# Optimization experiments

Hardware: AMD Instinct MI355X
Metric: run time of the kernel (lower is better)

Reference implementation:

```python
import jax, jax.numpy as jnp
import numpy as np

PS = 8  # window_size
LOCAL = 16  # split channels

def conv1x1(x, w, b):
    return jnp.einsum('oi,bihw->bohw', w, x) + b[None, :, None, None]

def dynamic_local(x, w1, b1, w2, b2, k):
    # x: (B, C, H, W); dynamic per-(batch,channel) depthwise conv with generated kernels
    B, C, H, W = x.shape
    pooled = x.mean((2, 3))                      # (B, C) adaptive avg pool to 1x1
    h = jax.nn.relu(pooled @ w1.T + b1)
    kern = (h @ w2.T + b2).reshape(B, C, k, k)   # per-sample depthwise kernels
    def per_batch(xb, kb):
        return jax.lax.conv_general_dilated(
            xb[None], kb[:, None], (1, 1), 'SAME',
            feature_group_count=C,
            dimension_numbers=('NCHW', 'OIHW', 'NCHW'))[0]
    return jax.vmap(per_batch)(x, kern)

def channel_layernorm(x, w, b, eps=1e-6):
    # LayerNorm over channel dim (torch module's non-channels_last path)
    u = x.mean(1, keepdims=True)
    s = ((x - u) ** 2).mean(1, keepdims=True)
    xn = (x - u) / jnp.sqrt(s + eps)
    return w[None, :, None, None] * xn + b[None, :, None, None]

def fsas(x, hid_w, hid_b, dw_w, dw_b, ln_w, ln_b, out_w, out_b):
    hidden = conv1x1(x, hid_w, hid_b)
    mid = hidden.shape[1]
    dw = jax.lax.conv_general_dilated(
        hidden, dw_w[:, None], (1, 1), 'SAME',
        feature_group_count=mid,
        dimension_numbers=('NCHW', 'OIHW', 'NCHW')) + dw_b[None, :, None, None]
    q, k, v = jnp.split(dw, 3, axis=1)
    B, C, H, W = q.shape
    def patch(t):
        # (B,C,H,W) -> (B,C,H/ps,W/ps,ps,ps)
        return t.reshape(B, C, H // PS, PS, W // PS, PS).transpose(0, 1, 2, 4, 3, 5)
    qf = jnp.fft.rfft2(patch(q))
    kf = jnp.fft.rfft2(patch(k))
    out = jnp.fft.irfft2(qf * kf, s=(PS, PS))
    out = out.transpose(0, 1, 2, 4, 3, 5).reshape(B, C, H, W)
    out = channel_layernorm(out, ln_w, ln_b)
    return conv1x1(v * out, out_w, out_b)


def setup_inputs() -> dict:
    key = jax.random.key(0)
    ks = jax.random.split(key, 12)
    s = 0.02
    return {
        'x': jax.random.normal(ks[0], (4, 64, 256, 256), jnp.float32),
        'dl1_w1': jax.random.normal(ks[1], (16, 16), jnp.float32) * s,
        'dl1_b1': jnp.zeros((16,), jnp.float32),
        'dl1_w2': jax.random.normal(ks[2], (144, 16), jnp.float32) * s,
        'dl1_b2': jnp.zeros((144,), jnp.float32),
        'dl2_w1': jax.random.normal(ks[3], (16, 16), jnp.float32) * s,
        'dl2_b1': jnp.zeros((16,), jnp.float32),
        'dl2_w2': jax.random.normal(ks[4], (400, 16), jnp.float32) * s,
        'dl2_b2': jnp.zeros((400,), jnp.float32),
        'fs_hid_w': jax.random.normal(ks[5], (144, 48), jnp.float32) * s,
        'fs_hid_b': jnp.zeros((144,), jnp.float32),
        'fs_dw_w': jax.random.normal(ks[6], (144, 3, 3), jnp.float32) * s,
        'fs_dw_b': jnp.zeros((144,), jnp.float32),
        'fs_ln_w': jnp.ones((48,), jnp.float32),
        'fs_ln_b': jnp.zeros((48,), jnp.float32),
        'fs_out_w': jax.random.normal(ks[7], (48, 48), jnp.float32) * s,
        'fs_out_b': jnp.zeros((48,), jnp.float32),
        'last_w': jax.random.normal(ks[8], (64, 64), jnp.float32) * s,
        'last_b': jnp.zeros((64,), jnp.float32),
    }


def reference(x, dl1_w1, dl1_b1, dl1_w2, dl1_b2, dl2_w1, dl2_b1, dl2_w2, dl2_b2,
              fs_hid_w, fs_hid_b, fs_dw_w, fs_dw_b, fs_ln_w, fs_ln_b,
              fs_out_w, fs_out_b, last_w, last_b):
    x1, x2 = x[:, :LOCAL], x[:, LOCAL:]
    x1 = dynamic_local(x1, dl1_w1, dl1_b1, dl1_w2, dl1_b2, 3)
    x1 = dynamic_local(x1, dl2_w1, dl2_b1, dl2_w2, dl2_b2, 5)
    x2 = fsas(x2, fs_hid_w, fs_hid_b, fs_dw_w, fs_dw_b, fs_ln_w, fs_ln_b, fs_out_w, fs_out_b)
    return conv1x1(jnp.concatenate([x1, x2], axis=1), last_w, last_b)
```

## Files before the change

kernel.cpp:

```cpp
#include <hip/hip_runtime.h>

typedef _Float16 h2 __attribute__((ext_vector_type(2)));
typedef _Float16 h4 __attribute__((ext_vector_type(4)));
typedef _Float16 h8 __attribute__((ext_vector_type(8)));
typedef float f4 __attribute__((ext_vector_type(4)));
typedef unsigned int u32;
typedef u32 u32x2 __attribute__((ext_vector_type(2)));
typedef u32 u32x4 __attribute__((ext_vector_type(4)));

__device__ __forceinline__ h2 bch2(u32 v) { return __builtin_bit_cast(h2, v); }

__device__ __forceinline__ float warpsum(float v) {
    for (int off = 32; off > 0; off >>= 1) v += __shfl_down(v, off);
    return v;
}

__device__ __forceinline__ int sswz(int p, int k) {
    return p * 64 + ((((k >> 3) ^ (p >> 3)) & 7) << 3) + (k & 7);
}

__global__ __launch_bounds__(256) void k_prep(const float* __restrict__ hid_w,
                                              const float* __restrict__ out_w,
                                              const float* __restrict__ last_w,
                                              const float* __restrict__ out_b,
                                              const float* __restrict__ last_b,
                                              _Float16* __restrict__ hwH,
                                              _Float16* __restrict__ lwC,
                                              float* __restrict__ bias_comb) {
    int t = blockIdx.x * 256 + threadIdx.x;
    int stride = gridDim.x * 256;
    for (int i = t; i < 10368; i += stride) {
        int n = i / 72, k = i - n * 72;
        hwH[i] = (k < 48) ? (_Float16)hid_w[n * 48 + k] : (_Float16)0.f;
    }
    for (int i = t; i < 4096; i += stride) {
        int n = i >> 6, k = i & 63;
        float v;
        if (k < 16) v = last_w[n * 64 + k];
        else {
            v = 0.f;
            for (int o = 0; o < 48; ++o) v += last_w[n * 64 + 16 + o] * out_w[o * 48 + (k - 16)];
        }
        lwC[i] = (_Float16)v;
    }
    for (int n = t; n < 64; n += stride) {
        float v = last_b[n];
        for (int o = 0; o < 48; ++o) v += last_w[n * 64 + 16 + o] * out_b[o];
        bias_comb[n] = v;
    }
}

__global__ __launch_bounds__(256) void k_pool(const float* __restrict__ x, float* __restrict__ pooled1) {
    int bid = blockIdx.x;
    int b = bid >> 4, c = bid & 15;
    const float* base = x + (size_t)(b * 64 + c) * 65536;
    float s = 0.f;
    for (int i = threadIdx.x; i < 16384; i += 256) {
        float4 v = ((const float4*)base)[i];
        s += v.x + v.y + v.z + v.w;
    }
    __shared__ float red[4];
    s = warpsum(s);
    if ((threadIdx.x & 63) == 0) red[threadIdx.x >> 6] = s;
    __syncthreads();
    if (threadIdx.x == 0) pooled1[bid] = (red[0] + red[1] + red[2] + red[3]) * (1.f / 65536.f);
}

__global__ __launch_bounds__(256) void k_kern1(const float* __restrict__ pooled1,
                                               const float* __restrict__ w1, const float* __restrict__ b1,
                                               const float* __restrict__ w2, const float* __restrict__ b2,
                                               float* __restrict__ kern1) {
    __shared__ float h[64];
    int t = threadIdx.x;
    if (t < 64) {
        int b = t >> 4, j = t & 15;
        float a = b1[j];
        for (int i = 0; i < 16; ++i) a += pooled1[b * 16 + i] * w1[j * 16 + i];
        h[t] = fmaxf(a, 0.f);
    }
    __syncthreads();
    for (int i = t; i < 576; i += 256) {
        int b = i / 144, o = i - b * 144;
        float a = b2[o];
        for (int j = 0; j < 16; ++j) a += h[b * 16 + j] * w2[o * 16 + j];
        kern1[i] = a;
    }
}

__global__ __launch_bounds__(256) void k_dw3(const float* __restrict__ x,
                                             const float* __restrict__ kern1,
                                             float* __restrict__ y1, float* __restrict__ rowsum) {
    __shared__ float tile[10][258];
    __shared__ float red[8][4];
    int bid = blockIdx.x;
    int rb = bid & 31, bc = bid >> 5;
    int b = bc >> 4, c = bc & 15;
    int row0 = rb << 3;
    int col = threadIdx.x;
    const float* xc = x + ((size_t)(b * 64 + c) << 16);
#pragma unroll
    for (int j = 0; j < 10; ++j) {
        int r = row0 - 1 + j;
        tile[j][col + 1] = ((unsigned)r < 256u) ? xc[(r << 8) + col] : 0.f;
    }
    if (col < 10) { tile[col][0] = 0.f; tile[col][257] = 0.f; }
    const float* k9 = kern1 + b * 144 + c * 9;
    float kk[9];
#pragma unroll
    for (int i = 0; i < 9; ++i) kk[i] = k9[i];
    __syncthreads();
#pragma unroll
    for (int j = 0; j < 8; ++j) {
        float acc = 0.f;
#pragma unroll
        for (int dy = 0; dy < 3; ++dy)
#pragma unroll
            for (int dx = 0; dx < 3; ++dx)
                acc += kk[dy * 3 + dx] * tile[j + dy][col + dx];
        y1[((size_t)bc << 16) + ((row0 + j) << 8) + col] = acc;
        float s = warpsum(acc);
        if ((col & 63) == 0) red[j][col >> 6] = s;
    }
    __syncthreads();
    if (col < 8) rowsum[bc * 256 + row0 + col] = red[col][0] + red[col][1] + red[col][2] + red[col][3];
}

__global__ __launch_bounds__(256) void k_kern2(const float* __restrict__ rowsum,
                                               const float* __restrict__ w1, const float* __restrict__ b1,
                                               const float* __restrict__ w2, const float* __restrict__ b2,
                                               float* __restrict__ kern2) {
    __shared__ float ps[256];
    __shared__ float p2[64];
    __shared__ float h[64];
    int t = threadIdx.x;
    {
        int pair = t >> 2, seg = t & 3;
        const float* rs = rowsum + pair * 256 + seg * 64;
        float s = 0.f;
        for (int j = 0; j < 64; ++j) s += rs[j];
        ps[t] = s;
    }
    __syncthreads();
    if (t < 64) p2[t] = (ps[t * 4] + ps[t * 4 + 1] + ps[t * 4 + 2] + ps[t * 4 + 3]) * (1.f / 65536.f);
    __syncthreads();
    if (t < 64) {
        int b = t >> 4, j = t & 15;
        float a = b1[j];
        for (int i = 0; i < 16; ++i) a += p2[b * 16 + i] * w1[j * 16 + i];
        h[t] = fmaxf(a, 0.f);
    }
    __syncthreads();
    for (int i = t; i < 1600; i += 256) {
        int b = i / 400, o = i - b * 400;
        float a = b2[o];
        for (int j = 0; j < 16; ++j) a += h[b * 16 + j] * w2[o * 16 + j];
        kern2[i] = a;
    }
}

__global__ __launch_bounds__(256) void k_dw5(const float* __restrict__ y1,
                                             const float* __restrict__ kern2,
                                             float* __restrict__ x1o) {
    __shared__ float tile[12][260];
    int bid = blockIdx.x;
    int rb = bid & 31, bc = bid >> 5;
    int b = bc >> 4, c = bc & 15;
    int row0 = rb << 3;
    int col = threadIdx.x;
    const float* yc = y1 + ((size_t)bc << 16);
#pragma unroll
    for (int j = 0; j < 12; ++j) {
        int r = row0 - 2 + j;
        tile[j][col + 2] = ((unsigned)r < 256u) ? yc[(r << 8) + col] : 0.f;
    }
    if (col < 12) { tile[col][0] = 0.f; tile[col][1] = 0.f; tile[col][258] = 0.f; tile[col][259] = 0.f; }
    const float* k25 = kern2 + b * 400 + c * 25;
    float kk[25];
#pragma unroll
    for (int i = 0; i < 25; ++i) kk[i] = k25[i];
    __syncthreads();
#pragma unroll
    for (int j = 0; j < 8; ++j) {
        float acc = 0.f;
#pragma unroll
        for (int dy = 0; dy < 5; ++dy)
#pragma unroll
            for (int dx = 0; dx < 5; ++dx)
                acc += kk[dy * 5 + dx] * tile[j + dy][col + dx];
        x1o[((size_t)bc << 16) + ((row0 + j) << 8) + col] = acc;
    }
}

__global__ __launch_bounds__(512, 6) void k_fsas(const float* __restrict__ x,
                                                 const _Float16* __restrict__ hwH, const float* __restrict__ hid_b,
                                                 const float* __restrict__ dw_w, const float* __restrict__ dw_b,
                                                 const float* __restrict__ ln_w, const float* __restrict__ ln_b,
                                                 const _Float16* __restrict__ lwC, const float* __restrict__ bias_comb,
                                                 const float* __restrict__ x1o, float* __restrict__ out) {
    __shared__ __align__(16) _Float16 Sbig[17856];
    __shared__ __align__(16) _Float16 qk[6144];

    _Float16* Abuf = Sbig;
    _Float16* hbuf = Sbig;
    _Float16* fbuf = Sbig;
    float*    lnp2 = (float*)(Sbig + 4608);
    _Float16* qbuf = qk;
    _Float16* kbuf = qk + 3072;

    int tid = threadIdx.x;
    int lane = tid & 63;
    int wave = __builtin_amdgcn_readfirstlane(tid >> 6);
    int bid = blockIdx.x;
    int swz = ((bid & 7) << 9) | (bid >> 3);
    int b = swz >> 10;
    int rem = swz & 1023;
    int row0 = (rem >> 5) << 3, col0 = (rem & 31) << 3;

    int l16 = lane & 15, lhi = lane >> 4;
    int mb = wave * 16 + (lhi << 2);
    bool vok[4];
#pragma unroll
    for (int r = 0; r < 4; ++r) {
        int m = mb + r;
        int yv = m / 12, xv = m - yv * 12;
        vok[r] = (m < 120) && (xv < 10) &&
                 ((unsigned)(row0 - 1 + yv) < 256u) && ((unsigned)(col0 - 1 + xv) < 256u);
    }

    if (tid < 480) {
        int k2 = tid / 20, r20 = tid - (tid / 20) * 20;
        int y = r20 >> 1, xh = r20 & 1;
        int gy = row0 - 1 + y;
        bool rowok = (unsigned)gy < 256u;
        const float* xa = x + ((size_t)(b * 64 + 16 + 2 * k2) << 16) + ((size_t)(gy & 255) << 8);
        const float* xb = xa + 65536;
#pragma unroll
        for (int xx = 0; xx < 6; ++xx) {
            int xv = xh * 6 + xx;
            int gx = col0 - 1 + xv;
            bool ok = rowok && (xv < 10) && ((unsigned)gx < 256u);
            float va = ok ? xa[gx] : 0.f;
            float vb = ok ? xb[gx] : 0.f;
            *(h2*)(Abuf + (y * 12 + xv) * 72 + 2 * k2) = (h2){(_Float16)va, (_Float16)vb};
        }
    }
    if (tid < 240) {
        int p = tid >> 1, kb = 48 + ((tid & 1) << 3);
        *(h8*)(Abuf + p * 72 + kb) = (h8)(_Float16)0.f;
    }
    __syncthreads();

    int arow = wave * 16 + l16;
    h8 a0 = *(const h8*)(Abuf + arow * 72 + (lhi << 3));
    h8 a1 = *(const h8*)(Abuf + arow * 72 + 32 + (lhi << 3));
    __syncthreads();

    float xr[8];
    int fgrp = wave - 6;
    if (wave >= 6) {
        size_t gp = ((size_t)(row0 + (lane >> 3)) << 8) + col0 + (lane & 7);
#pragma unroll
        for (int j = 0; j < 8; ++j)
            xr[j] = x1o[((size_t)(b * 16 + fgrp * 8 + j) << 16) + gp];
    }

#pragma unroll
    for (int nt = 0; nt < 9; ++nt) {
        const _Float16* wr = hwH + (nt * 16 + l16) * 72 + (lhi << 3);
        h8 b0 = *(const h8*)(wr);
        h8 b1 = *(const h8*)(wr + 32);
        float bias = hid_b[nt * 16 + l16];
        f4 acc = {bias, bias, bias, bias};
        acc = __builtin_amdgcn_mfma_f32_16x16x32_f16(a0, b0, acc, 0, 0, 0);
        acc = __builtin_amdgcn_mfma_f32_16x16x32_f16(a1, b1, acc, 0, 0, 0);
        int n_l = nt * 16 + l16;
        if (mb < 120) {
            h2 p0 = {vok[0] ? (_Float16)acc[0] : (_Float16)0.f, vok[1] ? (_Float16)acc[1] : (_Float16)0.f};
            h2 p1 = {vok[2] ? (_Float16)acc[2] : (_Float16)0.f, vok[3] ? (_Float16)acc[3] : (_Float16)0.f};
            *(h2*)(hbuf + n_l * 124 + mb) = p0;
            *(h2*)(hbuf + n_l * 124 + mb + 2) = p1;
        }
    }
    __syncthreads();

    int dch = tid >> 3, drow = tid & 7;
    h8 vreg;
    auto dw_row = [&](int ch, int row, float o[8]) {
        const float* dwp = dw_w + ch * 9;
        float bias = dw_b[ch];
#pragma unroll
        for (int xx = 0; xx < 8; ++xx) o[xx] = bias;
        const _Float16* hb = hbuf + ch * 124 + row * 12;
#pragma unroll
        for (int dy = 0; dy < 3; ++dy) {
            u32x2 A2 = *(const u32x2*)(hb + dy * 12);
            u32x2 B2 = *(const u32x2*)(hb + dy * 12 + 4);
            u32 r89 = *(const u32*)(hb + dy * 12 + 8);
            u32 r01 = A2.x, r23 = A2.y, r45 = B2.x, r67 = B2.y;
            u32 s12 = __builtin_amdgcn_alignbit(r23, r01, 16);
            u32 s34 = __builtin_amdgcn_alignbit(r45, r23, 16);
            u32 s56 = __builtin_amdgcn_alignbit(r67, r45, 16);
            u32 s78 = __builtin_amdgcn_alignbit(r89, r67, 16);
            _Float16 w0 = (_Float16)dwp[dy * 3], w1 = (_Float16)dwp[dy * 3 + 1], w2 = (_Float16)dwp[dy * 3 + 2];
            h2 w01 = {w0, w1};
            h2 w2lo = {w2, (_Float16)0.f};
            h2 w2hi = {(_Float16)0.f, w2};
            o[0] = __builtin_amdgcn_fdot2(w01, bch2(r01), o[0], false);
            o[0] = __builtin_amdgcn_fdot2(w2lo, bch2(r23), o[0], false);
            o[1] = __builtin_amdgcn_fdot2(w01, bch2(s12), o[1], false);
            o[1] = __builtin_amdgcn_fdot2(w2lo, bch2(s34), o[1], false);
            o[2] = __builtin_amdgcn_fdot2(w01, bch2(r23), o[2], false);
            o[2] = __builtin_amdgcn_fdot2(w2lo, bch2(r45), o[2], false);
            o[3] = __builtin_amdgcn_fdot2(w01, bch2(s34), o[3], false);
            o[3] = __builtin_amdgcn_fdot2(w2lo, bch2(s56), o[3], false);
            o[4] = __builtin_amdgcn_fdot2(w01, bch2(r45), o[4], false);
            o[4] = __builtin_amdgcn_fdot2(w2lo, bch2(r67), o[4], false);
            o[5] = __builtin_amdgcn_fdot2(w01, bch2(s56), o[5], false);
            o[5] = __builtin_amdgcn_fdot2(w2lo, bch2(s78), o[5], false);
            o[6] = __builtin_amdgcn_fdot2(w01, bch2(r67), o[6], false);
            o[6] = __builtin_amdgcn_fdot2(w2lo, bch2(r89), o[6], false);
            o[7] = __builtin_amdgcn_fdot2(w01, bch2(s78), o[7], false);
            o[7] = __builtin_amdgcn_fdot2(w2hi, bch2(r89), o[7], false);
        }
    };
    if (tid < 384) {
        float oq[8];
        dw_row(dch, drow, oq);
        h8 qv;
#pragma unroll
        for (int xx = 0; xx < 8; ++xx) qv[xx] = (_Float16)oq[xx];
        *(h8*)(qbuf + dch * 64 + drow * 8) = qv;
        float ov[8];
        dw_row(96 + dch, drow, ov);
#pragma unroll
        for (int xx = 0; xx < 8; ++xx) vreg[xx] = (_Float16)ov[xx];
    } else {
        int j0 = (tid - 384) * 3;
#pragma unroll
        for (int i = 0; i < 3; ++i) {
            int j = j0 + i;
            int kc = j >> 3, kr = j & 7;
            float ok8[8];
            dw_row(48 + kc, kr, ok8);
            h8 krv;
#pragma unroll
            for (int t2 = 0; t2 < 8; ++t2) krv[t2] = (_Float16)ok8[(8 - t2) & 7];
            *(h8*)(kbuf + kc * 64 + kr * 8) = krv;
        }
    }
    __syncthreads();

    float co[8];
    if (tid < 384) {
        int ch = dch, m = drow;
#pragma unroll
        for (int n = 0; n < 8; ++n) co[n] = 0.f;
#pragma unroll
        for (int i8 = 0; i8 < 8; ++i8) {
            int r = (m - i8) & 7;
            u32x4 qv = *(const u32x4*)(qbuf + ch * 64 + i8 * 8);
            u32x4 ev = *(const u32x4*)(kbuf + ch * 64 + r * 8);
            h2 qp[4] = {bch2(qv.x), bch2(qv.y), bch2(qv.z), bch2(qv.w)};
            h2 ep[4] = {bch2(ev.x), bch2(ev.y), bch2(ev.z), bch2(ev.w)};
            h2 op[4] = {bch2(__builtin_amdgcn_alignbit(ev.x, ev.w, 16)),
                        bch2(__builtin_amdgcn_alignbit(ev.y, ev.x, 16)),
                        bch2(__builtin_amdgcn_alignbit(ev.z, ev.y, 16)),
                        bch2(__builtin_amdgcn_alignbit(ev.w, ev.z, 16))};
#pragma unroll
            for (int u = 0; u < 4; ++u)
#pragma unroll
                for (int a = 0; a < 4; ++a) {
                    co[2 * u]     = __builtin_amdgcn_fdot2(qp[a], ep[(a - u) & 3], co[2 * u], false);
                    co[2 * u + 1] = __builtin_amdgcn_fdot2(qp[a], op[(a - u) & 3], co[2 * u + 1], false);
                }
        }
        float s[8], ss[8];
#pragma unroll
        for (int n = 0; n < 8; ++n) { s[n] = co[n]; ss[n] = co[n] * co[n]; }
#pragma unroll
        for (int off = 8; off < 64; off <<= 1) {
#pragma unroll
            for (int n = 0; n < 8; ++n) {
                s[n] += __shfl_xor(s[n], off);
                ss[n] += __shfl_xor(ss[n], off);
            }
        }
        int c8 = lane >> 3, mm = lane & 7;
        int p = mm * 8 + c8;
        float2 pv = {0.f, 0.f};
#pragma unroll
        for (int n = 0; n < 8; ++n) if (n == c8) { pv.x = s[n]; pv.y = ss[n]; }
        *(float2*)(lnp2 + wave * 128 + p * 2) = pv;
    } else {
        h8 fv;
#pragma unroll
        for (int j = 0; j < 8; ++j) fv[j] = (_Float16)xr[j];
        *(h8*)(fbuf + sswz(lane, fgrp * 8)) = fv;
    }
    __syncthreads();

    if (tid < 384) {
        int m = drow;
        float sAcc[8], ssAcc[8];
#pragma unroll
        for (int n = 0; n < 8; ++n) { sAcc[n] = 0.f; ssAcc[n] = 0.f; }
#pragma unroll
        for (int w = 0; w < 6; ++w) {
            const float* lp = lnp2 + w * 128 + m * 16;
#pragma unroll
            for (int j = 0; j < 4; ++j) {
                f4 v4 = *(const f4*)(lp + j * 4);
                sAcc[2 * j] += v4[0];  ssAcc[2 * j] += v4[1];
                sAcc[2 * j + 1] += v4[2]; ssAcc[2 * j + 1] += v4[3];
            }
        }
        float lw = ln_w[dch], lb = ln_b[dch];
#pragma unroll
        for (int n = 0; n < 8; ++n) {
            float mu = sAcc[n] * (1.f / 48.f);
            float var = ssAcc[n] * (1.f / 48.f) - mu * mu;
            float inv = rsqrtf(var + 1e-6f);
            float lnv = lw * ((co[n] - mu) * inv) + lb;
            fbuf[sswz(m * 8 + n, 16 + dch)] = (_Float16)((float)vreg[n] * lnv);
        }
    }
    __syncthreads();

    for (int t = wave; t < 16; t += 8) {
        int mt = t >> 2, nt = t & 3;
        int row6 = mt * 16 + l16;
        h8 c0 = *(const h8*)(fbuf + sswz(row6, lhi << 3));
        h8 c1 = *(const h8*)(fbuf + sswz(row6, 32 + (lhi << 3)));
        h8 d0 = *(const h8*)(lwC + (nt * 16 + l16) * 64 + (lhi << 3));
        h8 d1 = *(const h8*)(lwC + (nt * 16 + l16) * 64 + 32 + (lhi << 3));
        float bias = bias_comb[nt * 16 + l16];
        f4 acc = {bias, bias, bias, bias};
        acc = __builtin_amdgcn_mfma_f32_16x16x32_f16(c0, d0, acc, 0, 0, 0);
        acc = __builtin_amdgcn_mfma_f32_16x16x32_f16(c1, d1, acc, 0, 0, 0);
        int ch = nt * 16 + l16;
        int px0 = mt * 16 + (lhi << 2);
        float4 val = {acc[0], acc[1], acc[2], acc[3]};
        *(float4*)(out + ((size_t)(b * 64 + ch) << 16) + ((size_t)(row0 + (px0 >> 3)) << 8) + col0 + (px0 & 7)) = val;
    }
}

extern "C" void kernel_launch(void* const* d_in, const int* in_sizes, int n_in,
                              void* d_out, int out_size, void* d_ws, size_t ws_size,
                              hipStream_t stream) {
    const float* x      = (const float*)d_in[0];
    const float* dl1_w1 = (const float*)d_in[1];
    const float* dl1_b1 = (const float*)d_in[2];
    const float* dl1_w2 = (const float*)d_in[3];
    const float* dl1_b2 = (const float*)d_in[4];
    const float* dl2_w1 = (const float*)d_in[5];
    const float* dl2_b1 = (const float*)d_in[6];
    const float* dl2_w2 = (const float*)d_in[7];
    const float* dl2_b2 = (const float*)d_in[8];
    const float* hid_w  = (const float*)d_in[9];
    const float* hid_b  = (const float*)d_in[10];
    const float* dw_w   = (const float*)d_in[11];
    const float* dw_b   = (const float*)d_in[12];
    const float* ln_w   = (const float*)d_in[13];
    const float* ln_b   = (const float*)d_in[14];
    const float* out_w  = (const float*)d_in[15];
    const float* out_b  = (const float*)d_in[16];
    const float* last_w = (const float*)d_in[17];
    const float* last_b = (const float*)d_in[18];
    float* out = (float*)d_out;

    float* ws      = (float*)d_ws;
    float* pooled1 = ws;
    float* kern1   = ws + 64;
    float* rowsum  = ws + 1024;
    float* kern2   = ws + 17408;
    _Float16* hwH   = (_Float16*)(ws + 19008);
    _Float16* lwC   = (_Float16*)(ws + 24192);
    float* bias_comb = ws + 26240;
    float* y1      = ws + 32768;
    float* x1o     = ws + 32768 + 4194304;

    k_prep <<<8,    256, 0, stream>>>(hid_w, out_w, last_w, out_b, last_b, hwH, lwC, bias_comb);
    k_pool <<<64,   256, 0, stream>>>(x, pooled1);
    k_kern1<<<1,    256, 0, stream>>>(pooled1, dl1_w1, dl1_b1, dl1_w2, dl1_b2, kern1);
    k_dw3  <<<2048, 256, 0, stream>>>(x, kern1, y1, rowsum);
    k_kern2<<<1,    256, 0, stream>>>(rowsum, dl2_w1, dl2_b1, dl2_w2, dl2_b2, kern2);
    k_dw5  <<<2048, 256, 0, stream>>>(y1, kern2, x1o);
    k_fsas <<<4096, 512, 0, stream>>>(x, hwH, hid_b, dw_w, dw_b, ln_w, ln_b,
                                      lwC, bias_comb, x1o, out);
}
```

Before: 184.2 us.

## Stage swizzled hidden weights in LDS and compute layernorm stats via shared buffer

The prep kernel now writes the 144x48 hidden conv weights as a 64-wide, XOR-swizzled fp16 layout. Each fsas block copies it into LDS (reusing the q/k buffer, enlarged to 9216 halves) so the MFMA B-operands come from shared memory instead of global. The per-pixel channel layernorm statistics no longer use per-wave shuffle reductions; values are written as fp16 to a shared buffer and reduced in two block-wide passes into a mean/rsqrt table. Launch bounds drop from 6 to 4 blocks per CU, which relaxes register pressure but may lower occupancy, and the extra LDS traffic and syncs add cost.

```diff
diff --git a/kernel.cpp b/kernel.cpp
--- a/kernel.cpp
+++ b/kernel.cpp
@@ -24,14 +24,16 @@
                                               const float* __restrict__ last_w,
                                               const float* __restrict__ out_b,
                                               const float* __restrict__ last_b,
-                                              _Float16* __restrict__ hwH,
+                                              _Float16* __restrict__ hwP2,
                                               _Float16* __restrict__ lwC,
                                               float* __restrict__ bias_comb) {
     int t = blockIdx.x * 256 + threadIdx.x;
     int stride = gridDim.x * 256;
-    for (int i = t; i < 10368; i += stride) {
-        int n = i / 72, k = i - n * 72;
-        hwH[i] = (k < 48) ? (_Float16)hid_w[n * 48 + k] : (_Float16)0.f;
+    for (int i = t; i < 9216; i += stride) {
+        int n = i >> 6, r = i & 63;
+        int sb = r >> 3, kl = r & 7;
+        int k = (((sb ^ (n & 7)) & 7) << 3) + kl;
+        hwP2[i] = (k < 48) ? (_Float16)hid_w[n * 48 + k] : (_Float16)0.f;
     }
     for (int i = t; i < 4096; i += stride) {
         int n = i >> 6, k = i & 63;
@@ -191,21 +193,24 @@
     }
 }
 
-__global__ __launch_bounds__(512, 6) void k_fsas(const float* __restrict__ x,
-                                                 const _Float16* __restrict__ hwH, const float* __restrict__ hid_b,
+__global__ __launch_bounds__(512, 4) void k_fsas(const float* __restrict__ x,
+                                                 const _Float16* __restrict__ hwP2, const float* __restrict__ hid_b,
                                                  const float* __restrict__ dw_w, const float* __restrict__ dw_b,
                                                  const float* __restrict__ ln_w, const float* __restrict__ ln_b,
                                                  const _Float16* __restrict__ lwC, const float* __restrict__ bias_comb,
                                                  const float* __restrict__ x1o, float* __restrict__ out) {
     __shared__ __align__(16) _Float16 Sbig[17856];
-    __shared__ __align__(16) _Float16 qk[6144];
+    __shared__ __align__(16) _Float16 wq[9216];
 
     _Float16* Abuf = Sbig;
     _Float16* hbuf = Sbig;
     _Float16* fbuf = Sbig;
-    float*    lnp2 = (float*)(Sbig + 4608);
-    _Float16* qbuf = qk;
-    _Float16* kbuf = qk + 3072;
+    float*    lnp  = (float*)(Sbig + 4608);
+    _Float16* outb = Sbig + 6656;
+    float*    pstat = (float*)(Sbig + 9824);
+    _Float16* wbuf = wq;
+    _Float16* qbuf = wq;
+    _Float16* kbuf = wq + 3072;
 
     int tid = threadIdx.x;
     int lane = tid & 63;
@@ -248,6 +253,11 @@
         int p = tid >> 1, kb = 48 + ((tid & 1) << 3);
         *(h8*)(Abuf + p * 72 + kb) = (h8)(_Float16)0.f;
     }
+    {
+        const u32x4* srcw = (const u32x4*)hwP2;
+        u32x4* dstw = (u32x4*)wbuf;
+        for (int i = tid; i < 1152; i += 512) dstw[i] = srcw[i];
+    }
     __syncthreads();
 
     int arow = wave * 16 + l16;
@@ -266,14 +276,14 @@
 
 #pragma unroll
     for (int nt = 0; nt < 9; ++nt) {
-        const _Float16* wr = hwH + (nt * 16 + l16) * 72 + (lhi << 3);
-        h8 b0 = *(const h8*)(wr);
-        h8 b1 = *(const h8*)(wr + 32);
-        float bias = hid_b[nt * 16 + l16];
+        int n_l = nt * 16 + l16;
+        const _Float16* wr = wbuf + n_l * 64;
+        h8 b0 = *(const h8*)(wr + (((lhi ^ (n_l & 7)) & 7) << 3));
+        h8 b1 = *(const h8*)(wr + ((((lhi + 4) ^ (n_l & 7)) & 7) << 3));
+        float bias = hid_b[n_l];
         f4 acc = {bias, bias, bias, bias};
         acc = __builtin_amdgcn_mfma_f32_16x16x32_f16(a0, b0, acc, 0, 0, 0);
         acc = __builtin_amdgcn_mfma_f32_16x16x32_f16(a1, b1, acc, 0, 0, 0);
-        int n_l = nt * 16 + l16;
         if (mb < 120) {
             h2 p0 = {vok[0] ? (_Float16)acc[0] : (_Float16)0.f, vok[1] ? (_Float16)acc[1] : (_Float16)0.f};
             h2 p1 = {vok[2] ? (_Float16)acc[2] : (_Float16)0.f, vok[3] ? (_Float16)acc[3] : (_Float16)0.f};
@@ -374,23 +384,9 @@
                     co[2 * u + 1] = __builtin_amdgcn_fdot2(qp[a], op[(a - u) & 3], co[2 * u + 1], false);
                 }
         }
-        float s[8], ss[8];
-#pragma unroll
-        for (int n = 0; n < 8; ++n) { s[n] = co[n]; ss[n] = co[n] * co[n]; }
-#pragma unroll
-        for (int off = 8; off < 64; off <<= 1) {
-#pragma unroll
-            for (int n = 0; n < 8; ++n) {
-                s[n] += __shfl_xor(s[n], off);
-                ss[n] += __shfl_xor(ss[n], off);
-            }
-        }
-        int c8 = lane >> 3, mm = lane & 7;
-        int p = mm * 8 + c8;
-        float2 pv = {0.f, 0.f};
-#pragma unroll
-        for (int n = 0; n < 8; ++n) if (n == c8) { pv.x = s[n]; pv.y = ss[n]; }
-        *(float2*)(lnp2 + wave * 128 + p * 2) = pv;
+#pragma unroll
+        for (int v = 0; v < 4; ++v)
+            *(h2*)(outb + dch * 66 + drow * 8 + 2 * v) = (h2){(_Float16)co[2 * v], (_Float16)co[2 * v + 1]};
     } else {
         h8 fv;
 #pragma unroll
@@ -399,29 +395,37 @@
     }
     __syncthreads();
 
+    {
+        int px = tid & 63, g = tid >> 6;
+        float s = 0.f, ss = 0.f;
+#pragma unroll
+        for (int cc = 0; cc < 6; ++cc) {
+            float v = (float)outb[(g * 6 + cc) * 66 + px];
+            s += v; ss += v * v;
+        }
+        lnp[g * 64 + px] = s;
+        lnp[512 + g * 64 + px] = ss;
+    }
+    __syncthreads();
+    if (tid < 64) {
+        float s = 0.f, ss = 0.f;
+#pragma unroll
+        for (int g = 0; g < 8; ++g) { s += lnp[g * 64 + tid]; ss += lnp[512 + g * 64 + tid]; }
+        float mu = s * (1.f / 48.f);
+        float var = ss * (1.f / 48.f) - mu * mu;
+        pstat[tid * 2] = mu;
+        pstat[tid * 2 + 1] = rsqrtf(var + 1e-6f);
+    }
+    __syncthreads();
+
     if (tid < 384) {
-        int m = drow;
-        float sAcc[8], ssAcc[8];
-#pragma unroll
-        for (int n = 0; n < 8; ++n) { sAcc[n] = 0.f; ssAcc[n] = 0.f; }
-#pragma unroll
-        for (int w = 0; w < 6; ++w) {
-            const float* lp = lnp2 + w * 128 + m * 16;
-#pragma unroll
-            for (int j = 0; j < 4; ++j) {
-                f4 v4 = *(const f4*)(lp + j * 4);
-                sAcc[2 * j] += v4[0];  ssAcc[2 * j] += v4[1];
-                sAcc[2 * j + 1] += v4[2]; ssAcc[2 * j + 1] += v4[3];
-            }
-        }
         float lw = ln_w[dch], lb = ln_b[dch];
+        const float* ps = pstat + drow * 16;
 #pragma unroll
         for (int n = 0; n < 8; ++n) {
-            float mu = sAcc[n] * (1.f / 48.f);
-            float var = ssAcc[n] * (1.f / 48.f) - mu * mu;
-            float inv = rsqrtf(var + 1e-6f);
+            float mu = ps[2 * n], inv = ps[2 * n + 1];
             float lnv = lw * ((co[n] - mu) * inv) + lb;
-            fbuf[sswz(m * 8 + n, 16 + dch)] = (_Float16)((float)vreg[n] * lnv);
+            fbuf[sswz(drow * 8 + n, 16 + dch)] = (_Float16)((float)vreg[n] * lnv);
         }
     }
     __syncthreads();
@@ -473,18 +477,18 @@
     float* kern1   = ws + 64;
     float* rowsum  = ws + 1024;
     float* kern2   = ws + 17408;
-    _Float16* hwH   = (_Float16*)(ws + 19008);
-    _Float16* lwC   = (_Float16*)(ws + 24192);
-    float* bias_comb = ws + 26240;
+    _Float16* hwP2  = (_Float16*)(ws + 19008);
+    _Float16* lwC   = (_Float16*)(ws + 23616);
+    float* bias_comb = ws + 25664;
     float* y1      = ws + 32768;
     float* x1o     = ws + 32768 + 4194304;
 
-    k_prep <<<8,    256, 0, stream>>>(hid_w, out_w, last_w, out_b, last_b, hwH, lwC, bias_comb);
+    k_prep <<<8,    256, 0, stream>>>(hid_w, out_w, last_w, out_b, last_b, hwP2, lwC, bias_comb);
     k_pool <<<64,   256, 0, stream>>>(x, pooled1);
     k_kern1<<<1,    256, 0, stream>>>(pooled1, dl1_w1, dl1_b1, dl1_w2, dl1_b2, kern1);
     k_dw3  <<<2048, 256, 0, stream>>>(x, kern1, y1, rowsum);
     k_kern2<<<1,    256, 0, stream>>>(rowsum, dl2_w1, dl2_b1, dl2_w2, dl2_b2, kern2);
     k_dw5  <<<2048, 256, 0, stream>>>(y1, kern2, x1o);
-    k_fsas <<<4096, 512, 0, stream>>>(x, hwH, hid_b, dw_w, dw_b, ln_w, ln_b,
+    k_fsas <<<4096, 512, 0, stream>>>(x, hwP2, hid_b, dw_w, dw_b, ln_w, ln_b,
                                       lwC, bias_comb, x1o, out);
 }
```

After: 182.4 us. No clear change (-1.0%).

## Restructure FSAS kernel so waves own channel slices and drop block barriers

Applied to the files above, without the earlier changes.

The hidden projection now puts the weights in the MFMA A operand and the pixels in the B operand. Each wave writes its own 16 hidden channels, so the depthwise conv reads only wave-local data and the barrier between the projection and the conv goes away. The q/k/v depthwise results are written in place into the hidden buffer, and the leftover channels are computed by idle lanes during the FFT-correlation stage. The per-wave LayerNorm partials are replaced by LDS atomics plus one normalisation pass. The separate buffers raise LDS use per block, which may cut occupancy, and the atomics add contention.

```diff
diff --git a/kernel.cpp b/kernel.cpp
--- a/kernel.cpp
+++ b/kernel.cpp
@@ -197,15 +197,11 @@
                                                  const float* __restrict__ ln_w, const float* __restrict__ ln_b,
                                                  const _Float16* __restrict__ lwC, const float* __restrict__ bias_comb,
                                                  const float* __restrict__ x1o, float* __restrict__ out) {
-    __shared__ __align__(16) _Float16 Sbig[17856];
-    __shared__ __align__(16) _Float16 qk[6144];
-
-    _Float16* Abuf = Sbig;
-    _Float16* hbuf = Sbig;
-    _Float16* fbuf = Sbig;
-    float*    lnp2 = (float*)(Sbig + 4608);
-    _Float16* qbuf = qk;
-    _Float16* kbuf = qk + 3072;
+    __shared__ __align__(16) _Float16 Abuf[9216];
+    __shared__ __align__(16) _Float16 hbuf[17280];
+    __shared__ __align__(16) float lnp[128];
+
+    _Float16* fbuf = Abuf;
 
     int tid = threadIdx.x;
     int lane = tid & 63;
@@ -217,14 +213,14 @@
     int row0 = (rem >> 5) << 3, col0 = (rem & 31) << 3;
 
     int l16 = lane & 15, lhi = lane >> 4;
-    int mb = wave * 16 + (lhi << 2);
-    bool vok[4];
-#pragma unroll
-    for (int r = 0; r < 4; ++r) {
-        int m = mb + r;
-        int yv = m / 12, xv = m - yv * 12;
-        vok[r] = (m < 120) && (xv < 10) &&
-                 ((unsigned)(row0 - 1 + yv) < 256u) && ((unsigned)(col0 - 1 + xv) < 256u);
+
+    float xr[8];
+    int fgrp = wave - 6;
+    if (wave >= 6) {
+        size_t gp = ((size_t)(row0 + (lane >> 3)) << 8) + col0 + (lane & 7);
+#pragma unroll
+        for (int j = 0; j < 8; ++j)
+            xr[j] = x1o[((size_t)(b * 16 + fgrp * 8 + j) << 16) + gp];
     }
 
     if (tid < 480) {
@@ -244,53 +240,60 @@
             *(h2*)(Abuf + (y * 12 + xv) * 72 + 2 * k2) = (h2){(_Float16)va, (_Float16)vb};
         }
     }
-    if (tid < 240) {
+    if (tid < 256) {
         int p = tid >> 1, kb = 48 + ((tid & 1) << 3);
         *(h8*)(Abuf + p * 72 + kb) = (h8)(_Float16)0.f;
     }
-    __syncthreads();
-
-    int arow = wave * 16 + l16;
-    h8 a0 = *(const h8*)(Abuf + arow * 72 + (lhi << 3));
-    h8 a1 = *(const h8*)(Abuf + arow * 72 + 32 + (lhi << 3));
-    __syncthreads();
-
-    float xr[8];
-    int fgrp = wave - 6;
-    if (wave >= 6) {
-        size_t gp = ((size_t)(row0 + (lane >> 3)) << 8) + col0 + (lane & 7);
-#pragma unroll
-        for (int j = 0; j < 8; ++j)
-            xr[j] = x1o[((size_t)(b * 16 + fgrp * 8 + j) << 16) + gp];
-    }
-
-#pragma unroll
-    for (int nt = 0; nt < 9; ++nt) {
-        const _Float16* wr = hwH + (nt * 16 + l16) * 72 + (lhi << 3);
-        h8 b0 = *(const h8*)(wr);
-        h8 b1 = *(const h8*)(wr + 32);
-        float bias = hid_b[nt * 16 + l16];
-        f4 acc = {bias, bias, bias, bias};
-        acc = __builtin_amdgcn_mfma_f32_16x16x32_f16(a0, b0, acc, 0, 0, 0);
-        acc = __builtin_amdgcn_mfma_f32_16x16x32_f16(a1, b1, acc, 0, 0, 0);
-        int n_l = nt * 16 + l16;
-        if (mb < 120) {
-            h2 p0 = {vok[0] ? (_Float16)acc[0] : (_Float16)0.f, vok[1] ? (_Float16)acc[1] : (_Float16)0.f};
-            h2 p1 = {vok[2] ? (_Float16)acc[2] : (_Float16)0.f, vok[3] ? (_Float16)acc[3] : (_Float16)0.f};
-            *(h2*)(hbuf + n_l * 124 + mb) = p0;
-            *(h2*)(hbuf + n_l * 124 + mb + 2) = p1;
-        }
-    }
-    __syncthreads();
-
-    int dch = tid >> 3, drow = tid & 7;
-    h8 vreg;
+    if (tid < 128) lnp[tid] = 0.f;
+    __syncthreads();
+
+    const _Float16* wrO = hwH + (wave * 16 + l16) * 72 + (lhi << 3);
+    h8 wa0 = *(const h8*)(wrO);
+    h8 wa1 = *(const h8*)(wrO + 32);
+    const _Float16* wr8 = hwH + (128 + l16) * 72 + (lhi << 3);
+    h8 w80 = *(const h8*)(wr8);
+    h8 w81 = *(const h8*)(wr8 + 32);
+    f4 biasO = *(const f4*)(hid_b + wave * 16 + (lhi << 2));
+    f4 bias8 = *(const f4*)(hid_b + 128 + (lhi << 2));
+    int chbO = wave * 16 + (lhi << 2);
+    h8 xbs0, xbs1;
+#pragma unroll
+    for (int nt = 0; nt < 8; ++nt) {
+        int px = nt * 16 + l16;
+        h8 xb0 = *(const h8*)(Abuf + px * 72 + (lhi << 3));
+        h8 xb1 = *(const h8*)(Abuf + px * 72 + 32 + (lhi << 3));
+        if (nt == wave) { xbs0 = xb0; xbs1 = xb1; }
+        f4 acc = biasO;
+        acc = __builtin_amdgcn_mfma_f32_16x16x32_f16(wa0, xb0, acc, 0, 0, 0);
+        acc = __builtin_amdgcn_mfma_f32_16x16x32_f16(wa1, xb1, acc, 0, 0, 0);
+        if (px < 120) {
+            int yv = px / 12, xv = px - yv * 12;
+            bool ok = (xv < 10) && ((unsigned)(row0 - 1 + yv) < 256u) && ((unsigned)(col0 - 1 + xv) < 256u);
+#pragma unroll
+            for (int r = 0; r < 4; ++r)
+                hbuf[(chbO + r) * 120 + px] = ok ? (_Float16)acc[r] : (_Float16)0.f;
+        }
+    }
+    {
+        int px = wave * 16 + l16;
+        f4 acc = bias8;
+        acc = __builtin_amdgcn_mfma_f32_16x16x32_f16(w80, xbs0, acc, 0, 0, 0);
+        acc = __builtin_amdgcn_mfma_f32_16x16x32_f16(w81, xbs1, acc, 0, 0, 0);
+        if (px < 120) {
+            int yv = px / 12, xv = px - yv * 12;
+            bool ok = (xv < 10) && ((unsigned)(row0 - 1 + yv) < 256u) && ((unsigned)(col0 - 1 + xv) < 256u);
+#pragma unroll
+            for (int r = 0; r < 4; ++r)
+                hbuf[(128 + (lhi << 2) + r) * 120 + px] = ok ? (_Float16)acc[r] : (_Float16)0.f;
+        }
+    }
+
     auto dw_row = [&](int ch, int row, float o[8]) {
         const float* dwp = dw_w + ch * 9;
         float bias = dw_b[ch];
 #pragma unroll
         for (int xx = 0; xx < 8; ++xx) o[xx] = bias;
-        const _Float16* hb = hbuf + ch * 124 + row * 12;
+        const _Float16* hb = hbuf + ch * 120 + row * 12;
 #pragma unroll
         for (int dy = 0; dy < 3; ++dy) {
             u32x2 A2 = *(const u32x2*)(hb + dy * 12);
@@ -323,43 +326,39 @@
             o[7] = __builtin_amdgcn_fdot2(w2hi, bch2(r89), o[7], false);
         }
     };
-    if (tid < 384) {
-        float oq[8];
-        dw_row(dch, drow, oq);
-        h8 qv;
-#pragma unroll
-        for (int xx = 0; xx < 8; ++xx) qv[xx] = (_Float16)oq[xx];
-        *(h8*)(qbuf + dch * 64 + drow * 8) = qv;
-        float ov[8];
-        dw_row(96 + dch, drow, ov);
-#pragma unroll
-        for (int xx = 0; xx < 8; ++xx) vreg[xx] = (_Float16)ov[xx];
-    } else {
-        int j0 = (tid - 384) * 3;
-#pragma unroll
-        for (int i = 0; i < 3; ++i) {
-            int j = j0 + i;
-            int kc = j >> 3, kr = j & 7;
-            float ok8[8];
-            dw_row(48 + kc, kr, ok8);
-            h8 krv;
-#pragma unroll
-            for (int t2 = 0; t2 < 8; ++t2) krv[t2] = (_Float16)ok8[(8 - t2) & 7];
-            *(h8*)(kbuf + kc * 64 + kr * 8) = krv;
-        }
+    auto route_write = [&](int c, int m, float o[8]) {
+        h8 v8;
+        if (c >= 48 && c < 96) {
+#pragma unroll
+            for (int t2 = 0; t2 < 8; ++t2) v8[t2] = (_Float16)o[(8 - t2) & 7];
+        } else {
+#pragma unroll
+            for (int t2 = 0; t2 < 8; ++t2) v8[t2] = (_Float16)o[t2];
+        }
+        *(h8*)(hbuf + c * 120 + m * 8) = v8;
+    };
+    {
+        int c1 = wave * 16 + (lane >> 3), m1 = lane & 7;
+        int c2 = wave * 16 + 8 + (lane >> 3), m2 = lane & 7;
+        float o1[8], o2[8];
+        dw_row(c1, m1, o1);
+        dw_row(c2, m2, o2);
+        route_write(c1, m1, o1);
+        route_write(c2, m2, o2);
     }
     __syncthreads();
 
     float co[8];
-    if (tid < 384) {
-        int ch = dch, m = drow;
+    int cch = wave * 6 + (lane >> 3);
+    int cm = lane & 7;
+    if (lane < 48) {
 #pragma unroll
         for (int n = 0; n < 8; ++n) co[n] = 0.f;
 #pragma unroll
         for (int i8 = 0; i8 < 8; ++i8) {
-            int r = (m - i8) & 7;
-            u32x4 qv = *(const u32x4*)(qbuf + ch * 64 + i8 * 8);
-            u32x4 ev = *(const u32x4*)(kbuf + ch * 64 + r * 8);
+            int r = (cm - i8) & 7;
+            u32x4 qv = *(const u32x4*)(hbuf + cch * 120 + i8 * 8);
+            u32x4 ev = *(const u32x4*)(hbuf + (48 + cch) * 120 + r * 8);
             h2 qp[4] = {bch2(qv.x), bch2(qv.y), bch2(qv.z), bch2(qv.w)};
             h2 ep[4] = {bch2(ev.x), bch2(ev.y), bch2(ev.z), bch2(ev.w)};
             h2 op[4] = {bch2(__builtin_amdgcn_alignbit(ev.x, ev.w, 16)),
@@ -374,6 +373,19 @@
                     co[2 * u + 1] = __builtin_amdgcn_fdot2(qp[a], op[(a - u) & 3], co[2 * u + 1], false);
                 }
         }
+    } else {
+        int c8 = 128 + wave * 2 + ((lane >> 3) & 1);
+        int m8 = lane & 7;
+        float o8v[8];
+        dw_row(c8, m8, o8v);
+        h8 v8;
+#pragma unroll
+        for (int t2 = 0; t2 < 8; ++t2) v8[t2] = (_Float16)o8v[t2];
+        *(h8*)(hbuf + c8 * 120 + m8 * 8) = v8;
+#pragma unroll
+        for (int n = 0; n < 8; ++n) co[n] = 0.f;
+    }
+    {
         float s[8], ss[8];
 #pragma unroll
         for (int n = 0; n < 8; ++n) { s[n] = co[n]; ss[n] = co[n] * co[n]; }
@@ -385,44 +397,41 @@
                 ss[n] += __shfl_xor(ss[n], off);
             }
         }
-        int c8 = lane >> 3, mm = lane & 7;
-        int p = mm * 8 + c8;
-        float2 pv = {0.f, 0.f};
-#pragma unroll
-        for (int n = 0; n < 8; ++n) if (n == c8) { pv.x = s[n]; pv.y = ss[n]; }
-        *(float2*)(lnp2 + wave * 128 + p * 2) = pv;
-    } else {
+        if (lane < 8) {
+#pragma unroll
+            for (int n = 0; n < 8; ++n) {
+                atomicAdd(&lnp[(lane * 8 + n) * 2], s[n]);
+                atomicAdd(&lnp[(lane * 8 + n) * 2 + 1], ss[n]);
+            }
+        }
+    }
+    __syncthreads();
+
+    if (tid < 64) {
+        float sv = lnp[tid * 2], ssv = lnp[tid * 2 + 1];
+        float mu = sv * (1.f / 48.f);
+        float var = ssv * (1.f / 48.f) - mu * mu;
+        lnp[tid * 2] = mu;
+        lnp[tid * 2 + 1] = rsqrtf(var + 1e-6f);
+    }
+    __syncthreads();
+
+    if (lane < 48) {
+        float lw = ln_w[cch], lb = ln_b[cch];
+        h8 vv = *(const h8*)(hbuf + (96 + cch) * 120 + cm * 8);
+#pragma unroll
+        for (int n = 0; n < 8; ++n) {
+            int p = cm * 8 + n;
+            float mu = lnp[p * 2], inv = lnp[p * 2 + 1];
+            float lnv = lw * ((co[n] - mu) * inv) + lb;
+            fbuf[sswz(p, 16 + cch)] = (_Float16)((float)vv[n] * lnv);
+        }
+    }
+    if (wave >= 6) {
         h8 fv;
 #pragma unroll
         for (int j = 0; j < 8; ++j) fv[j] = (_Float16)xr[j];
         *(h8*)(fbuf + sswz(lane, fgrp * 8)) = fv;
-    }
-    __syncthreads();
-
-    if (tid < 384) {
-        int m = drow;
-        float sAcc[8], ssAcc[8];
-#pragma unroll
-        for (int n = 0; n < 8; ++n) { sAcc[n] = 0.f; ssAcc[n] = 0.f; }
-#pragma unroll
-        for (int w = 0; w < 6; ++w) {
-            const float* lp = lnp2 + w * 128 + m * 16;
-#pragma unroll
-            for (int j = 0; j < 4; ++j) {
-                f4 v4 = *(const f4*)(lp + j * 4);
-                sAcc[2 * j] += v4[0];  ssAcc[2 * j] += v4[1];
-                sAcc[2 * j + 1] += v4[2]; ssAcc[2 * j + 1] += v4[3];
-            }
-        }
-        float lw = ln_w[dch], lb = ln_b[dch];
-#pragma unroll
-        for (int n = 0; n < 8; ++n) {
-            float mu = sAcc[n] * (1.f / 48.f);
-            float var = ssAcc[n] * (1.f / 48.f) - mu * mu;
-            float inv = rsqrtf(var + 1e-6f);
-            float lnv = lw * ((co[n] - mu) * inv) + lb;
-            fbuf[sswz(m * 8 + n, 16 + dch)] = (_Float16)((float)vreg[n] * lnv);
-        }
     }
     __syncthreads();
 
```

After: 213.6 us. 1.16x slower.
